# Performance work log

Hardware: AMD Instinct MI355X
Metric: run time of the kernel (lower is better)

## Reference

```python
import math
import jax, jax.numpy as jnp
import numpy as np

B, S, D, H = 4, 2048, 1024, 16
DK = D // H
THETA = 10000.0


def _rope(xh, pos):
    # xh: [B, H, S, DK], pos: [S]
    half = jnp.arange(0, DK, 2, dtype=jnp.float32) / DK
    inv_freq = THETA ** (-half)                      # [DK/2]
    ang = pos.astype(jnp.float32)[:, None] * inv_freq  # [S, DK/2]
    cos, sin = jnp.cos(ang).astype(xh.dtype), jnp.sin(ang).astype(xh.dtype)
    x1, x2 = xh[..., 0::2], xh[..., 1::2]
    r1 = x1 * cos - x2 * sin
    r2 = x1 * sin + x2 * cos
    return jnp.stack([r1, r2], axis=-1).reshape(xh.shape)


def setup_inputs() -> dict:
    key = jax.random.key(0)
    kx, kq, kk, kv, ko = jax.random.split(key, 5)
    std = 0.02
    x = jax.random.normal(kx, (B, S, D), jnp.float32)
    wq = jax.random.normal(kq, (D, D), jnp.float32) * std
    wk = jax.random.normal(kk, (D, D), jnp.float32) * std
    wv = jax.random.normal(kv, (D, D), jnp.float32) * std
    wo = jax.random.normal(ko, (D, D), jnp.float32) * std
    token_positions = jnp.arange(S, dtype=jnp.int32)
    return {"x": x, "wq": wq, "wk": wk, "wv": wv, "wo": wo,
            "token_positions": token_positions}


def reference(x, wq, wk, wv, wo, token_positions):
    # bias-free linear projections: y = x @ W^T (torch Linear convention)
    q = x @ wq.T
    k = x @ wk.T
    v = x @ wv.T
    # split heads: [B, S, D] -> [B, H, S, DK]
    to_heads = lambda t: t.reshape(B, S, H, DK).transpose(0, 2, 1, 3)
    qh, kh, vh = to_heads(q), to_heads(k), to_heads(v)
    qh = _rope(qh, token_positions)
    kh = _rope(kh, token_positions)
    scores = jnp.einsum('bhqd,bhkd->bhqk', qh, kh) / math.sqrt(DK)
    causal = jnp.tril(jnp.ones((S, S), dtype=bool))
    scores = jnp.where(causal, scores, -jnp.inf)
    attn = jax.nn.softmax(scores, axis=-1)
    out = jnp.einsum('bhqk,bhkd->bhqd', attn, vh)       # [B, H, S, DK]
    out = out.transpose(0, 2, 1, 3).reshape(B, S, D)    # merge heads
    return out @ wo.T
```

## Files before the change

kernel.cpp:

```cpp
#include <hip/hip_runtime.h>

#define B_ 4
#define S_ 2048
#define D_ 1024
#define H_ 16
#define DK_ 64
#define M_ (B_*S_)
#define K_ D_
#define N_ D_
#define NSTEP 32

typedef unsigned short u16;
typedef unsigned int u32;
typedef __bf16 bf16x8 __attribute__((ext_vector_type(8)));
typedef float f32x4 __attribute__((ext_vector_type(4)));
typedef u32 u32x4v __attribute__((ext_vector_type(4)));

#define EXP2F(x) __builtin_amdgcn_exp2f(x)

__device__ __forceinline__ u16 f2bf(float f) {
    u32 u = __builtin_bit_cast(u32, f);
    u += 0x7fff + ((u >> 16) & 1);
    return (u16)(u >> 16);
}
__device__ __forceinline__ float bf2f(u16 h) {
    u32 u = ((u32)h) << 16;
    return __builtin_bit_cast(float, u);
}
__device__ __forceinline__ u32 pack_trunc(float a, float b) {
    return (__builtin_bit_cast(u32, a) >> 16) | (__builtin_bit_cast(u32, b) & 0xffff0000u);
}

#define GLDS16(g, l) __builtin_amdgcn_global_load_lds( \
    (__attribute__((address_space(1))) void*)(g),      \
    (__attribute__((address_space(3))) void*)(l), 16, 0, 0)

__global__ __launch_bounds__(256) void cvt_x(const float* __restrict__ in,
                                             u16* __restrict__ out, int n4) {
    const int i = blockIdx.x * 256 + threadIdx.x;
    if (i >= n4) return;
    const float4 f = *(const float4*)(in + (size_t)i * 4);
    u32 p0 = (u32)f2bf(f.x) | ((u32)f2bf(f.y) << 16);
    u32 p1 = (u32)f2bf(f.z) | ((u32)f2bf(f.w) << 16);
    *(uint2*)(out + (size_t)i * 4) = make_uint2(p0, p1);
}

__global__ __launch_bounds__(256) void cvt_w4(
    const float* __restrict__ w0, const float* __restrict__ w1,
    const float* __restrict__ w2, const float* __restrict__ w3,
    u16* __restrict__ o0, u16* __restrict__ o1,
    u16* __restrict__ o2, u16* __restrict__ o3) {
    const int wi = blockIdx.y;
    const float* in = (wi == 0) ? w0 : (wi == 1) ? w1 : (wi == 2) ? w2 : w3;
    u16* out       = (wi == 0) ? o0 : (wi == 1) ? o1 : (wi == 2) ? o2 : o3;
    const int i = blockIdx.x * 256 + threadIdx.x;
    const float4 f = *(const float4*)(in + (size_t)i * 4);
    u32 p0 = (u32)f2bf(f.x) | ((u32)f2bf(f.y) << 16);
    u32 p1 = (u32)f2bf(f.z) | ((u32)f2bf(f.w) << 16);
    *(uint2*)(out + (size_t)i * 4) = make_uint2(p0, p1);
}

template <int MODE>
__device__ __forceinline__ void gemm_tile(const u16* __restrict__ A,
                                          const u16* __restrict__ Bm,
                                          void* __restrict__ Cv,
                                          int m0, int n0,
                                          u16* __restrict__ As,
                                          u16* __restrict__ Bs) {
    const int tid  = threadIdx.x;
    const int wave = tid >> 6, lane = tid & 63;
    const int wm = wave & 1, wn = wave >> 1;
    const int quad = lane >> 4, mcol = lane & 15;

    const int c0 = wave, c1 = wave + 4;
    const int r0 = c0 * 16 + (lane >> 2), r1 = c1 * 16 + (lane >> 2);
    const int kb = (((lane & 3) ^ ((lane >> 3) & 3)) * 8);
    const u16* ga0 = A  + (size_t)(m0 + r0) * K_ + kb;
    const u16* ga1 = A  + (size_t)(m0 + r1) * K_ + kb;
    const u16* gb0 = Bm + (size_t)(n0 + r0) * K_ + kb;
    const u16* gb1 = Bm + (size_t)(n0 + r1) * K_ + kb;
    const int lo0 = c0 * 512, lo1 = c1 * 512;
    const int rsw = ((mcol >> 1) & 3);

    f32x4 acc[4][4];
#pragma unroll
    for (int i = 0; i < 4; i++)
#pragma unroll
        for (int j = 0; j < 4; j++) acc[i][j] = f32x4{0.f, 0.f, 0.f, 0.f};

    GLDS16(ga0, As + lo0); GLDS16(ga1, As + lo1);
    GLDS16(gb0, Bs + lo0); GLDS16(gb1, Bs + lo1);
    ga0 += 32; ga1 += 32; gb0 += 32; gb1 += 32;
    GLDS16(ga0, As + 4096 + lo0); GLDS16(ga1, As + 4096 + lo1);
    GLDS16(gb0, Bs + 4096 + lo0); GLDS16(gb1, Bs + 4096 + lo1);
    ga0 += 32; ga1 += 32; gb0 += 32; gb1 += 32;

    int cur = 0, tgt = 2;
    for (int t = 0; t < NSTEP; ++t) {
        if (t < NSTEP - 1) asm volatile("s_waitcnt vmcnt(4)" ::: "memory");
        else               asm volatile("s_waitcnt vmcnt(0)" ::: "memory");
        asm volatile("s_waitcnt lgkmcnt(0)" ::: "memory");
        __builtin_amdgcn_s_barrier();

        if (t < NSTEP - 2) {
            u16* at = As + tgt * 4096;
            u16* bt = Bs + tgt * 4096;
            GLDS16(ga0, at + lo0); GLDS16(ga1, at + lo1);
            GLDS16(gb0, bt + lo0); GLDS16(gb1, bt + lo1);
            ga0 += 32; ga1 += 32; gb0 += 32; gb1 += 32;
        }

        const u16* Ab = As + cur * 4096;
        const u16* Bb = Bs + cur * 4096;
        bf16x8 af[4], bfr[4];
#pragma unroll
        for (int i = 0; i < 4; i++) {
            af[i]  = *(const bf16x8*)&Ab[(wm * 64 + i * 16 + mcol) * 32 + (quad ^ rsw) * 8];
            bfr[i] = *(const bf16x8*)&Bb[(wn * 64 + i * 16 + mcol) * 32 + (quad ^ rsw) * 8];
        }
        __builtin_amdgcn_s_setprio(1);
#pragma unroll
        for (int i = 0; i < 4; i++)
#pragma unroll
            for (int j = 0; j < 4; j++)
                acc[i][j] = __builtin_amdgcn_mfma_f32_16x16x32_bf16(
                    af[i], bfr[j], acc[i][j], 0, 0, 0);
        __builtin_amdgcn_s_setprio(0);

        cur = (cur == 2) ? 0 : cur + 1;
        tgt = (tgt == 2) ? 0 : tgt + 1;
    }

#pragma unroll
    for (int i = 0; i < 4; i++) {
        const int row = m0 + wm * 64 + i * 16 + quad * 4;
#pragma unroll
        for (int j = 0; j < 4; j++) {
            const int col = n0 + wn * 64 + j * 16 + mcol;
            if constexpr (MODE == 2) {
                const int hh = col >> 6, dd = col & 63;
                const int bb = row >> 11, ss = row & 2047;
                const u32 lo = (u32)f2bf(acc[i][j][0]) | ((u32)f2bf(acc[i][j][1]) << 16);
                const u32 hi = (u32)f2bf(acc[i][j][2]) | ((u32)f2bf(acc[i][j][3]) << 16);
                *(uint2*)((u16*)Cv + ((size_t)((bb * H_ + hh) * DK_ + dd)) * S_ + ss) =
                    make_uint2(lo, hi);
            } else {
#pragma unroll
                for (int r = 0; r < 4; r++) {
                    if constexpr (MODE == 1)
                        ((float*)Cv)[(size_t)(row + r) * N_ + col] = acc[i][j][r];
                    else
                        ((u16*)Cv)[(size_t)(row + r) * N_ + col] = f2bf(acc[i][j][r]);
                }
            }
        }
    }
}

__global__ __launch_bounds__(256) void gemm_qkv_kernel(
    const u16* __restrict__ x,
    const u16* __restrict__ wq, const u16* __restrict__ wk,
    const u16* __restrict__ wv,
    u16* __restrict__ q, u16* __restrict__ k, u16* __restrict__ vt) {
    __shared__ u16 As[3 * 4096];
    __shared__ u16 Bs[3 * 4096];
    const int flat = blockIdx.x;
    const int w = (flat & 7) * 192 + (flat >> 3);
    const int my = w / 24;
    const int rem = w - my * 24;
    const int z = rem >> 3, nx = rem & 7;
    const int m0 = my * 128, n0 = nx * 128;
    if (z == 2) {
        gemm_tile<2>(x, wv, vt, m0, n0, As, Bs);
    } else {
        const u16* Bm = z ? wk : wq;
        u16* C        = z ? k  : q;
        gemm_tile<0>(x, Bm, C, m0, n0, As, Bs);
    }
}

__global__ __launch_bounds__(256) void gemm_out_kernel(
    const u16* __restrict__ o, const u16* __restrict__ wo, float* __restrict__ out) {
    __shared__ u16 As[3 * 4096];
    __shared__ u16 Bs[3 * 4096];
    const int flat = blockIdx.x;
    const int w = (flat & 7) * 64 + (flat >> 3);
    const int my = w >> 3, nx = w & 7;
    gemm_tile<1>(o, wo, out, my * 128, nx * 128, As, Bs);
}

__global__ __launch_bounds__(256) void rope_qk(u16* __restrict__ q,
                                               u16* __restrict__ k,
                                               const int* __restrict__ pos) {
    const int idx = blockIdx.x * 256 + threadIdx.x;
    const int seg = idx & 3;
    const int h = (idx >> 2) & (H_ - 1);
    const int s = (idx >> 6) & (S_ - 1);
    const int b = idx >> 17;
    const float p = (float)pos[s];
    const float QSC = 0.18033688011112042f;
    const size_t off = ((size_t)(b * S_ + s)) * D_ + h * DK_ + seg * 16;

    u32 qa[8], ka[8];
    *(uint4*)&qa[0] = *(const uint4*)(q + off);
    *(uint4*)&qa[4] = *(const uint4*)(q + off + 8);
    *(uint4*)&ka[0] = *(const uint4*)(k + off);
    *(uint4*)&ka[4] = *(const uint4*)(k + off + 8);
#pragma unroll
    for (int w = 0; w < 8; w++) {
        const int i = seg * 8 + w;
        const float inv = exp2f((float)i * (-13.287712379549449f / 32.f));
        const float ang = p * inv;
        float sn, cs;
        __sincosf(ang, &sn, &cs);
        {
            const float x1 = bf2f((u16)(qa[w] & 0xffff));
            const float x2 = bf2f((u16)(qa[w] >> 16));
            qa[w] = (u32)f2bf((x1 * cs - x2 * sn) * QSC) |
                    ((u32)f2bf((x1 * sn + x2 * cs) * QSC) << 16);
        }
        {
            const float x1 = bf2f((u16)(ka[w] & 0xffff));
            const float x2 = bf2f((u16)(ka[w] >> 16));
            ka[w] = (u32)f2bf(x1 * cs - x2 * sn) |
                    ((u32)f2bf(x1 * sn + x2 * cs) << 16);
        }
    }
    *(uint4*)(q + off)     = *(uint4*)&qa[0];
    *(uint4*)(q + off + 8) = *(uint4*)&qa[4];
    *(uint4*)(k + off)     = *(uint4*)&ka[0];
    *(uint4*)(k + off + 8) = *(uint4*)&ka[4];
}

__global__ __launch_bounds__(256) void attn_kernel(
    const u16* __restrict__ q, const u16* __restrict__ k,
    const u16* __restrict__ vt, u16* __restrict__ o) {
    __shared__ u16 Ks[64 * 64];
    __shared__ u16 Vs[64 * 64];

    const int tid = threadIdx.x, wave = tid >> 6, lane = tid & 63;
    const int flat = blockIdx.x;
    const int qp = flat >> 6;
    const int h = flat & (H_ - 1);
    const int b = (flat >> 4) & 3;
    const int quad = lane >> 4, mcol = lane & 15;
    const int srd = mcol & 7;

    const int rr2 = tid >> 2, cc2 = tid & 3;
    const int sw = rr2 & 7;
    const int so0 = rr2 * 64 + (((cc2 * 2)     ^ sw) << 3);
    const int so1 = rr2 * 64 + (((cc2 * 2 + 1) ^ sw) << 3);
    const int prr = (rr2 & 35) | ((rr2 & 12) << 1) | ((rr2 & 16) >> 2);
    const int ch2 = cc2 * 16;
    const u16* krow = k + ((size_t)(b * S_ + prr)) * D_ + h * DK_ + ch2;
    const u16* vrow = vt + ((size_t)((b * H_ + h) * DK_ + rr2)) * S_ + ch2;

    u32x4v onesw;
    onesw[0] = onesw[1] = onesw[2] = onesw[3] = 0x3F803F80u;
    const bf16x8 onesf = __builtin_bit_cast(bf16x8, onesw);

    for (int pass = 0; pass < 2; pass++) {
        const int qt = pass ? (15 - qp) : qp;
        const int q0 = qt * 128;
        const int wq0 = q0 + wave * 32;
        const int jmax = 2 * qt + 1;

        bf16x8 qf[2][2];
#pragma unroll
        for (int g = 0; g < 2; g++) {
            const u16* qs = q + ((size_t)(b * S_ + wq0 + g * 16 + mcol)) * D_ + h * DK_ + quad * 8;
            qf[g][0] = *(const bf16x8*)qs;
            qf[g][1] = *(const bf16x8*)(qs + 32);
        }

        float m[2] = {-1e30f, -1e30f};
        f32x4 lacc[2];
        f32x4 oacc[2][4];
#pragma unroll
        for (int g = 0; g < 2; g++) {
            lacc[g] = f32x4{0.f, 0.f, 0.f, 0.f};
#pragma unroll
            for (int dn = 0; dn < 4; dn++) oacc[g][dn] = f32x4{0.f, 0.f, 0.f, 0.f};
        }

        uint4 kr0 = *(const uint4*)(krow);
        uint4 kr1 = *(const uint4*)(krow + 8);
        uint4 vr0 = *(const uint4*)(vrow);
        uint4 vr1 = *(const uint4*)(vrow + 8);

        for (int j = 0; j <= jmax; j++) {
            __syncthreads();
            *(uint4*)&Ks[so0] = kr0;
            *(uint4*)&Ks[so1] = kr1;
            *(uint4*)&Vs[so0] = vr0;
            *(uint4*)&Vs[so1] = vr1;
            __syncthreads();

            if (j < jmax) {
                kr0 = *(const uint4*)(krow + (size_t)(j + 1) * 64 * D_);
                kr1 = *(const uint4*)(krow + (size_t)(j + 1) * 64 * D_ + 8);
                vr0 = *(const uint4*)(vrow + (j + 1) * 64);
                vr1 = *(const uint4*)(vrow + (j + 1) * 64 + 8);
            }

            if (j * 64 > wq0 + 31) continue;

            f32x4 st[2][4];
            __builtin_amdgcn_s_setprio(1);
#pragma unroll
            for (int n = 0; n < 4; n++) {
                const u16* kl = &Ks[(n * 16 + mcol) * 64];
                bf16x8 kf0 = *(const bf16x8*)&kl[(quad ^ srd) << 3];
                bf16x8 kf1 = *(const bf16x8*)&kl[((quad | 4) ^ srd) << 3];
                f32x4 z0 = f32x4{0.f, 0.f, 0.f, 0.f};
                z0 = __builtin_amdgcn_mfma_f32_16x16x32_bf16(kf0, qf[0][0], z0, 0, 0, 0);
                z0 = __builtin_amdgcn_mfma_f32_16x16x32_bf16(kf1, qf[0][1], z0, 0, 0, 0);
                st[0][n] = z0;
                f32x4 z1 = f32x4{0.f, 0.f, 0.f, 0.f};
                z1 = __builtin_amdgcn_mfma_f32_16x16x32_bf16(kf0, qf[1][0], z1, 0, 0, 0);
                z1 = __builtin_amdgcn_mfma_f32_16x16x32_bf16(kf1, qf[1][1], z1, 0, 0, 0);
                st[1][n] = z1;
            }
            __builtin_amdgcn_s_setprio(0);

            if (j * 64 + 63 > wq0) {
#pragma unroll
                for (int g = 0; g < 2; g++) {
                    const int qg = wq0 + g * 16 + mcol;
#pragma unroll
                    for (int n = 0; n < 4; n++) {
                        const int tb = j * 64 + ((n >> 1) << 5) + ((n & 1) << 2) + quad * 8;
#pragma unroll
                        for (int r = 0; r < 4; r++)
                            if (tb + r > qg) st[g][n][r] = -1e30f;
                    }
                }
            }

#pragma unroll
            for (int g = 0; g < 2; g++) {
                float mx = st[g][0][0];
#pragma unroll
                for (int n = 0; n < 4; n++)
#pragma unroll
                    for (int r = 0; r < 4; r++) mx = fmaxf(mx, st[g][n][r]);
                mx = fmaxf(mx, __shfl_xor(mx, 16));
                mx = fmaxf(mx, __shfl_xor(mx, 32));
                const bool need = !__all(mx <= m[g] + 8.f);
                if (need) {
                    const float mnew = fmaxf(m[g], mx);
                    const float al = EXP2F(m[g] - mnew);
                    m[g] = mnew;
                    float alphaT[4];
#pragma unroll
                    for (int r = 0; r < 4; r++) alphaT[r] = __shfl(al, quad * 4 + r);
#pragma unroll
                    for (int dn = 0; dn < 4; dn++)
#pragma unroll
                        for (int r = 0; r < 4; r++) oacc[g][dn][r] *= alphaT[r];
#pragma unroll
                    for (int r = 0; r < 4; r++) lacc[g][r] *= alphaT[r];
                }
#pragma unroll
                for (int n = 0; n < 4; n++)
#pragma unroll
                    for (int r = 0; r < 4; r++)
                        st[g][n][r] = EXP2F(st[g][n][r] - m[g]);
            }

            bf16x8 pf[2][2];
#pragma unroll
            for (int g = 0; g < 2; g++) {
                u32x4v w0, w1;
                w0[0] = pack_trunc(st[g][0][0], st[g][0][1]);
                w0[1] = pack_trunc(st[g][0][2], st[g][0][3]);
                w0[2] = pack_trunc(st[g][1][0], st[g][1][1]);
                w0[3] = pack_trunc(st[g][1][2], st[g][1][3]);
                w1[0] = pack_trunc(st[g][2][0], st[g][2][1]);
                w1[1] = pack_trunc(st[g][2][2], st[g][2][3]);
                w1[2] = pack_trunc(st[g][3][0], st[g][3][1]);
                w1[3] = pack_trunc(st[g][3][2], st[g][3][3]);
                pf[g][0] = __builtin_bit_cast(bf16x8, w0);
                pf[g][1] = __builtin_bit_cast(bf16x8, w1);
            }

            __builtin_amdgcn_s_setprio(1);
#pragma unroll
            for (int g = 0; g < 2; g++) {
                lacc[g] = __builtin_amdgcn_mfma_f32_16x16x32_bf16(pf[g][0], onesf, lacc[g], 0, 0, 0);
                lacc[g] = __builtin_amdgcn_mfma_f32_16x16x32_bf16(pf[g][1], onesf, lacc[g], 0, 0, 0);
            }
#pragma unroll
            for (int dn = 0; dn < 4; dn++) {
                const u16* vl = &Vs[(dn * 16 + mcol) * 64];
                bf16x8 vf0 = *(const bf16x8*)&vl[(quad ^ srd) << 3];
                bf16x8 vf1 = *(const bf16x8*)&vl[((quad | 4) ^ srd) << 3];
#pragma unroll
                for (int g = 0; g < 2; g++) {
                    oacc[g][dn] = __builtin_amdgcn_mfma_f32_16x16x32_bf16(pf[g][0], vf0, oacc[g][dn], 0, 0, 0);
                    oacc[g][dn] = __builtin_amdgcn_mfma_f32_16x16x32_bf16(pf[g][1], vf1, oacc[g][dn], 0, 0, 0);
                }
            }
            __builtin_amdgcn_s_setprio(0);
        }

#pragma unroll
        for (int g = 0; g < 2; g++) {
            float linv[4];
#pragma unroll
            for (int r = 0; r < 4; r++) linv[r] = 1.f / lacc[g][r];
#pragma unroll
            for (int dn = 0; dn < 4; dn++)
#pragma unroll
                for (int r = 0; r < 4; r++) {
                    const int row = wq0 + g * 16 + quad * 4 + r;
                    o[((size_t)(b * S_ + row)) * D_ + h * DK_ + dn * 16 + mcol] =
                        f2bf(oacc[g][dn][r] * linv[r]);
                }
        }
    }
}

extern "C" void kernel_launch(void* const* d_in, const int* in_sizes, int n_in,
                              void* d_out, int out_size, void* d_ws, size_t ws_size,
                              hipStream_t stream) {
    const float* x  = (const float*)d_in[0];
    const float* wq = (const float*)d_in[1];
    const float* wk = (const float*)d_in[2];
    const float* wv = (const float*)d_in[3];
    const float* wo = (const float*)d_in[4];
    const int*   tp = (const int*)d_in[5];
    float* out = (float*)d_out;

    u16* ws = (u16*)d_ws;
    const size_t NE = (size_t)M_ * D_;
    const size_t WE = (size_t)N_ * K_;
    u16* xb  = ws;
    u16* wqb = ws + NE;
    u16* wkb = wqb + WE;
    u16* wvb = wkb + WE;
    u16* wob = wvb + WE;
    u16* qb  = wob + WE;
    u16* kb  = qb + NE;
    u16* vtb = (u16*)d_out;
    u16* ob  = xb;

    dim3 blk(256);
    cvt_x<<<dim3((int)(NE / 1024)), blk, 0, stream>>>(x, xb, (int)(NE / 4));
    cvt_w4<<<dim3((int)(WE / 1024), 4), blk, 0, stream>>>(wq, wk, wv, wo, wqb, wkb, wvb, wob);

    gemm_qkv_kernel<<<dim3(3 * (M_ / 128) * (N_ / 128)), blk, 0, stream>>>(xb, wqb, wkb, wvb, qb, kb, vtb);
    rope_qk<<<dim3((B_ * S_ * H_ * 4) / 256), blk, 0, stream>>>(qb, kb, tp);
    attn_kernel<<<dim3((S_ / 128 / 2) * H_ * B_), blk, 0, stream>>>(qb, kb, vtb, ob);
    gemm_out_kernel<<<dim3((M_ / 128) * (N_ / 128)), blk, 0, stream>>>(ob, wob, out);
}
```

Before: 260.5 us.

## Merge conversion kernels and switch GEMM to double-buffered LDS pipeline

```diff
diff --git a/kernel.cpp b/kernel.cpp
--- a/kernel.cpp
+++ b/kernel.cpp
@@ -35,29 +35,30 @@
     (__attribute__((address_space(1))) void*)(g),      \
     (__attribute__((address_space(3))) void*)(l), 16, 0, 0)
 
-__global__ __launch_bounds__(256) void cvt_x(const float* __restrict__ in,
-                                             u16* __restrict__ out, int n4) {
-    const int i = blockIdx.x * 256 + threadIdx.x;
-    if (i >= n4) return;
-    const float4 f = *(const float4*)(in + (size_t)i * 4);
+__global__ __launch_bounds__(256) void cvt_all(
+    const float* __restrict__ x,
+    const float* __restrict__ w0, const float* __restrict__ w1,
+    const float* __restrict__ w2, const float* __restrict__ w3,
+    u16* __restrict__ xb,
+    u16* __restrict__ o0, u16* __restrict__ o1,
+    u16* __restrict__ o2, u16* __restrict__ o3) {
+    const size_t i = (size_t)blockIdx.x * 256 + threadIdx.x;
+    const float* in;
+    u16* out;
+    size_t off;
+    if (i < 2097152) {
+        in = x; out = xb; off = i;
+    } else {
+        const size_t j = i - 2097152;
+        const int wi = (int)(j >> 18);
+        off = j & 262143;
+        in  = (wi == 0) ? w0 : (wi == 1) ? w1 : (wi == 2) ? w2 : w3;
+        out = (wi == 0) ? o0 : (wi == 1) ? o1 : (wi == 2) ? o2 : o3;
+    }
+    const float4 f = *(const float4*)(in + off * 4);
     u32 p0 = (u32)f2bf(f.x) | ((u32)f2bf(f.y) << 16);
     u32 p1 = (u32)f2bf(f.z) | ((u32)f2bf(f.w) << 16);
-    *(uint2*)(out + (size_t)i * 4) = make_uint2(p0, p1);
-}
-
-__global__ __launch_bounds__(256) void cvt_w4(
-    const float* __restrict__ w0, const float* __restrict__ w1,
-    const float* __restrict__ w2, const float* __restrict__ w3,
-    u16* __restrict__ o0, u16* __restrict__ o1,
-    u16* __restrict__ o2, u16* __restrict__ o3) {
-    const int wi = blockIdx.y;
-    const float* in = (wi == 0) ? w0 : (wi == 1) ? w1 : (wi == 2) ? w2 : w3;
-    u16* out       = (wi == 0) ? o0 : (wi == 1) ? o1 : (wi == 2) ? o2 : o3;
-    const int i = blockIdx.x * 256 + threadIdx.x;
-    const float4 f = *(const float4*)(in + (size_t)i * 4);
-    u32 p0 = (u32)f2bf(f.x) | ((u32)f2bf(f.y) << 16);
-    u32 p1 = (u32)f2bf(f.z) | ((u32)f2bf(f.w) << 16);
-    *(uint2*)(out + (size_t)i * 4) = make_uint2(p0, p1);
+    *(uint2*)(out + off * 4) = make_uint2(p0, p1);
 }
 
 template <int MODE>
@@ -91,20 +92,16 @@
     GLDS16(ga0, As + lo0); GLDS16(ga1, As + lo1);
     GLDS16(gb0, Bs + lo0); GLDS16(gb1, Bs + lo1);
     ga0 += 32; ga1 += 32; gb0 += 32; gb1 += 32;
-    GLDS16(ga0, As + 4096 + lo0); GLDS16(ga1, As + 4096 + lo1);
-    GLDS16(gb0, Bs + 4096 + lo0); GLDS16(gb1, Bs + 4096 + lo1);
-    ga0 += 32; ga1 += 32; gb0 += 32; gb1 += 32;
-
-    int cur = 0, tgt = 2;
+
+    int cur = 0;
     for (int t = 0; t < NSTEP; ++t) {
-        if (t < NSTEP - 1) asm volatile("s_waitcnt vmcnt(4)" ::: "memory");
-        else               asm volatile("s_waitcnt vmcnt(0)" ::: "memory");
+        asm volatile("s_waitcnt vmcnt(0)" ::: "memory");
         asm volatile("s_waitcnt lgkmcnt(0)" ::: "memory");
         __builtin_amdgcn_s_barrier();
 
-        if (t < NSTEP - 2) {
-            u16* at = As + tgt * 4096;
-            u16* bt = Bs + tgt * 4096;
+        if (t + 1 < NSTEP) {
+            u16* at = As + (cur ^ 1) * 4096;
+            u16* bt = Bs + (cur ^ 1) * 4096;
             GLDS16(ga0, at + lo0); GLDS16(ga1, at + lo1);
             GLDS16(gb0, bt + lo0); GLDS16(gb1, bt + lo1);
             ga0 += 32; ga1 += 32; gb0 += 32; gb1 += 32;
@@ -127,8 +124,7 @@
                     af[i], bfr[j], acc[i][j], 0, 0, 0);
         __builtin_amdgcn_s_setprio(0);
 
-        cur = (cur == 2) ? 0 : cur + 1;
-        tgt = (tgt == 2) ? 0 : tgt + 1;
+        cur ^= 1;
     }
 
 #pragma unroll
@@ -162,8 +158,8 @@
     const u16* __restrict__ wq, const u16* __restrict__ wk,
     const u16* __restrict__ wv,
     u16* __restrict__ q, u16* __restrict__ k, u16* __restrict__ vt) {
-    __shared__ u16 As[3 * 4096];
-    __shared__ u16 Bs[3 * 4096];
+    __shared__ u16 As[2 * 4096];
+    __shared__ u16 Bs[2 * 4096];
     const int flat = blockIdx.x;
     const int w = (flat & 7) * 192 + (flat >> 3);
     const int my = w / 24;
@@ -181,8 +177,8 @@
 
 __global__ __launch_bounds__(256) void gemm_out_kernel(
     const u16* __restrict__ o, const u16* __restrict__ wo, float* __restrict__ out) {
-    __shared__ u16 As[3 * 4096];
-    __shared__ u16 Bs[3 * 4096];
+    __shared__ u16 As[2 * 4096];
+    __shared__ u16 Bs[2 * 4096];
     const int flat = blockIdx.x;
     const int w = (flat & 7) * 64 + (flat >> 3);
     const int my = w >> 3, nx = w & 7;
@@ -446,8 +442,8 @@
     u16* ob  = xb;
 
     dim3 blk(256);
-    cvt_x<<<dim3((int)(NE / 1024)), blk, 0, stream>>>(x, xb, (int)(NE / 4));
-    cvt_w4<<<dim3((int)(WE / 1024), 4), blk, 0, stream>>>(wq, wk, wv, wo, wqb, wkb, wvb, wob);
+    cvt_all<<<dim3(12288), blk, 0, stream>>>(x, wq, wk, wv, wo,
+                                             xb, wqb, wkb, wvb, wob);
 
     gemm_qkv_kernel<<<dim3(3 * (M_ / 128) * (N_ / 128)), blk, 0, stream>>>(xb, wqb, wkb, wvb, qb, kb, vtb);
     rope_qk<<<dim3((B_ * S_ * H_ * 4) / 256), blk, 0, stream>>>(qb, kb, tp);
```

Result: no change. 259.5 us (-0.4%).
